# Optimization experiments

Hardware: AMD Instinct MI355X
Metric: run time of the kernel (lower is better)

Reference implementation:

```python
import jax, jax.numpy as jnp
import numpy as np

B, S, D, H = 4, 2048, 512, 8
HD = D // H  # head_size = 64


def setup_inputs() -> dict:
    key = jax.random.key(0)
    ks = jax.random.split(key, 11)
    sd = 1.0 / np.sqrt(D)
    return {
        "q": jax.random.normal(ks[0], (B, S, D), jnp.float32),
        "k": jax.random.normal(ks[1], (B, S, D), jnp.float32),
        "v": jax.random.normal(ks[2], (B, S, D), jnp.float32),
        "Wq": jax.random.normal(ks[3], (D, D), jnp.float32) * sd,
        "bq": jnp.zeros((D,), jnp.float32),
        "Wk": jax.random.normal(ks[4], (D, D), jnp.float32) * sd,
        "bk": jnp.zeros((D,), jnp.float32),
        "Wv": jax.random.normal(ks[5], (D, D), jnp.float32) * sd,
        "bv": jnp.zeros((D,), jnp.float32),
        "Wo": jax.random.normal(ks[6], (D, D), jnp.float32) * sd,
        "bo": jnp.zeros((D,), jnp.float32),
    }


def _split_heads(x):
    # [B,S,D] -> [B,H,S,HD]
    return x.reshape(B, S, H, HD).transpose(0, 2, 1, 3)


def reference(q, k, v, Wq, bq, Wk, bk, Wv, bv, Wo, bo):
    qp = _split_heads(q @ Wq.T + bq)
    kp = _split_heads(k @ Wk.T + bk)
    vp = _split_heads(v @ Wv.T + bv)
    scale = 1.0 / jnp.sqrt(jnp.float32(HD))
    scores = jnp.einsum("bhqd,bhkd->bhqk", qp, kp) * scale  # [B,H,S,S]
    weights = jax.nn.softmax(scores, axis=-1)
    ctx = jnp.einsum("bhqk,bhkd->bhqd", weights, vp)
    ctx = ctx.transpose(0, 2, 1, 3).reshape(B, S, D)
    return ctx @ Wo.T + bo
```

## Files before the change

kernel.cpp:

```cpp
#include <hip/hip_runtime.h>
#include <hip/hip_bf16.h>
#include <stdint.h>

#define BB   4
#define SS   2048
#define DDIM 512
#define HH   8
#define HDIM 64
#define MTOT (BB*SS)
#define QSCALE (0.125f * 1.44269504088896340736f)

typedef __bf16 bf16;
typedef __bf16 bf16x8 __attribute__((ext_vector_type(8)));
typedef float  f32x4  __attribute__((ext_vector_type(4)));

__device__ __forceinline__ f32x4 mfma32(bf16x8 a, bf16x8 b, f32x4 c) {
    return __builtin_amdgcn_mfma_f32_16x16x32_bf16(a, b, c, 0, 0, 0);
}

__device__ __forceinline__ void gload_lds16(const void* g, void* l) {
    __builtin_amdgcn_global_load_lds(
        (__attribute__((address_space(1))) unsigned int*)(uintptr_t)g,
        (__attribute__((address_space(3))) unsigned int*)l,
        16, 0, 0);
}

__device__ __forceinline__ short bf16bits(float f) {
    union { __bf16 h; short s; } u; u.h = (__bf16)f; return u.s;
}

__global__ void cvt_kernel(const float* __restrict__ q, const float* __restrict__ k,
                           const float* __restrict__ v, const float* __restrict__ w0,
                           const float* __restrict__ w1, const float* __restrict__ w2,
                           const float* __restrict__ w3,
                           bf16* __restrict__ dq, bf16* __restrict__ dk,
                           bf16* __restrict__ dv, bf16* __restrict__ dw0,
                           bf16* __restrict__ dw1, bf16* __restrict__ dw2,
                           bf16* __restrict__ dw3) {
    const float* s; bf16* d; int n4;
    switch (blockIdx.y) {
        case 0: s = q;  d = dq;  n4 = (BB*SS*DDIM)/4; break;
        case 1: s = k;  d = dk;  n4 = (BB*SS*DDIM)/4; break;
        case 2: s = v;  d = dv;  n4 = (BB*SS*DDIM)/4; break;
        case 3: s = w0; d = dw0; n4 = (DDIM*DDIM)/4; break;
        case 4: s = w1; d = dw1; n4 = (DDIM*DDIM)/4; break;
        case 5: s = w2; d = dw2; n4 = (DDIM*DDIM)/4; break;
        default: s = w3; d = dw3; n4 = (DDIM*DDIM)/4; break;
    }
    int stride = gridDim.x * blockDim.x;
    for (int i = blockIdx.x * blockDim.x + threadIdx.x; i < n4; i += stride) {
        float4 f = ((const float4*)s)[i];
        union { bf16 h[4]; uint2 u; } o;
        o.h[0] = (bf16)f.x; o.h[1] = (bf16)f.y; o.h[2] = (bf16)f.z; o.h[3] = (bf16)f.w;
        ((uint2*)d)[i] = o.u;
    }
}

#define GEMM_CORE(A_, W_, K_, MB_, NB_)                                          \
    __shared__ bf16 As[2][128 * 32];                                             \
    __shared__ bf16 Bs[2][128 * 32];                                             \
    const int tid = threadIdx.x;                                                 \
    const int w = tid >> 6, lane = tid & 63;                                     \
    const int c15 = lane & 15, quad = lane >> 4;                                 \
    const int mblk = (MB_), nblk = (NB_);                                        \
    const int wm = (w & 1) * 64, wn = (w >> 1) * 64;                             \
    f32x4 acc[4][4] = {};                                                        \
    const bf16* Ab = (A_) + (size_t)mblk * (K_);                                 \
    const bf16* Bb = (W_) + (size_t)nblk * (K_);                                 \
    int goff[2], soff[2];                                                        \
    _Pragma("unroll")                                                            \
    for (int ci = 0; ci < 2; ++ci) {                                             \
        const int s = (w * 2 + ci) * 64 + lane;                 \
        const int kr = s >> 2;                                                   \
        const int c = (s & 3) ^ ((kr >> 1) & 3);                                 \
        goff[ci] = kr * (K_) + c * 8;                                            \
        soff[ci] = s * 8;                                                        \
    }                                                                            \
    _Pragma("unroll")                                                            \
    for (int ci = 0; ci < 2; ++ci) {                                             \
        gload_lds16(Ab + goff[ci], &As[0][soff[ci]]);                            \
        gload_lds16(Bb + goff[ci], &Bs[0][soff[ci]]);                            \
    }                                                                            \
    int bufi = 0;                                                                \
    for (int kt = 0; kt < (K_); kt += 32) {                                      \
        __syncthreads();              \
        if (kt + 32 < (K_)) {                                                    \
            _Pragma("unroll")                                                    \
            for (int ci = 0; ci < 2; ++ci) {                                     \
                gload_lds16(Ab + goff[ci] + kt + 32, &As[bufi ^ 1][soff[ci]]);   \
                gload_lds16(Bb + goff[ci] + kt + 32, &Bs[bufi ^ 1][soff[ci]]);   \
            }                                                                    \
        }                                                                        \
        bf16x8 af[4], bfr[4];                                                    \
        _Pragma("unroll")                                                        \
        for (int i = 0; i < 4; ++i) {                                            \
            const int row = wm + i * 16 + c15;                                   \
            af[i] = *(const bf16x8*)&As[bufi][row * 32 + ((quad ^ ((row >> 1) & 3)) * 8)]; \
        }                                                                        \
        _Pragma("unroll")                                                        \
        for (int j = 0; j < 4; ++j) {                                            \
            const int row = wn + j * 16 + c15;                                   \
            bfr[j] = *(const bf16x8*)&Bs[bufi][row * 32 + ((quad ^ ((row >> 1) & 3)) * 8)]; \
        }                                                                        \
        _Pragma("unroll")                                                        \
        for (int i = 0; i < 4; ++i)                                              \
            _Pragma("unroll")                                                    \
            for (int j = 0; j < 4; ++j)                                          \
                acc[i][j] = mfma32(af[i], bfr[j], acc[i][j]);                    \
        bufi ^= 1;                                                               \
    }

__global__ __launch_bounds__(256, 4)
void proj_gemm(const bf16* __restrict__ qb, const bf16* __restrict__ kb,
               const bf16* __restrict__ vb,
               const bf16* __restrict__ Wq, const bf16* __restrict__ Wk,
               const bf16* __restrict__ Wv,
               const float* __restrict__ bq, const float* __restrict__ bk,
               const float* __restrict__ bv,
               bf16* __restrict__ Qp, bf16* __restrict__ Kp, bf16* __restrict__ Vt2) {
    const int mode = blockIdx.z;
    const bf16* A; const bf16* Wm; const float* bias;
    int mb, nb;
    if (mode == 0)      { A = qb; Wm = Wq; bias = bq; mb = blockIdx.x * 128; nb = blockIdx.y * 128; }
    else if (mode == 1) { A = kb; Wm = Wk; bias = bk; mb = blockIdx.x * 128; nb = blockIdx.y * 128; }
    else {
        const int id = blockIdx.y * 64 + blockIdx.x;
        A = Wv; Wm = vb; bias = bv; mb = (id & 3) * 128; nb = (id >> 2) * 128;
    }
    GEMM_CORE(A, Wm, DDIM, mb, nb)
    if (mode == 2) {
        #pragma unroll
        for (int i = 0; i < 4; ++i) {
            #pragma unroll
            for (int r = 0; r < 4; ++r) {
                const int row = mblk + wm + i * 16 + quad * 4 + r;
                const float bval = bias[row];
                #pragma unroll
                for (int j = 0; j < 4; ++j) {
                    const int col = nblk + wn + j * 16 + c15;
                    const int colp = (col & ~31) + (c15 >> 2) * 8 + (j & 1) * 4 + (c15 & 3);
                    Vt2[(size_t)row * MTOT + colp] = (bf16)(acc[i][j][r] + bval);
                }
            }
        }
    } else {
        #pragma unroll
        for (int j = 0; j < 4; ++j) {
            const int col = nblk + wn + j * 16 + c15;
            const int h = col >> 6, hd = col & 63;
            const float bval = bias[col];
            #pragma unroll
            for (int i = 0; i < 4; ++i) {
                #pragma unroll
                for (int r = 0; r < 4; ++r) {
                    const int row = mblk + wm + i * 16 + quad * 4 + r;
                    const int b = row >> 11, s = row & (SS - 1);
                    float vv = acc[i][j][r] + bval;
                    if (mode == 0) vv *= QSCALE;
                    bf16* dst = (mode == 0) ? Qp : Kp;
                    dst[(((size_t)(b * HH + h)) * SS + s) * HDIM + hd] = (bf16)vv;
                }
            }
        }
    }
}

__global__ __launch_bounds__(256, 4)
void out_gemm(const bf16* __restrict__ A, const bf16* __restrict__ Wo,
              const float* __restrict__ bo, float* __restrict__ Out) {
    __shared__ bf16 As[2][128 * 32];
    __shared__ bf16 Bs[2][64 * 32];
    const int tid = threadIdx.x;
    const int w = tid >> 6, lane = tid & 63;
    const int c15 = lane & 15, quad = lane >> 4;
    const int mblk = blockIdx.x * 128, nblk = blockIdx.y * 64;
    const int wm = (w & 1) * 64, wn = (w >> 1) * 32;
    f32x4 acc[4][2] = {};
    const bf16* Ab = A + (size_t)mblk * DDIM;
    const bf16* Bb = Wo + (size_t)nblk * DDIM;
    int goffA[2], soffA[2];
    #pragma unroll
    for (int ci = 0; ci < 2; ++ci) {
        const int s = (w * 2 + ci) * 64 + lane;
        const int kr = s >> 2;
        const int c = (s & 3) ^ ((kr >> 1) & 3);
        goffA[ci] = kr * DDIM + c * 8;
        soffA[ci] = s * 8;
    }
    const int sB = w * 64 + lane;
    const int krB = sB >> 2;
    const int cB = (sB & 3) ^ ((krB >> 1) & 3);
    const int goffB = krB * DDIM + cB * 8;
    const int soffB = sB * 8;

    #pragma unroll
    for (int ci = 0; ci < 2; ++ci)
        gload_lds16(Ab + goffA[ci], &As[0][soffA[ci]]);
    gload_lds16(Bb + goffB, &Bs[0][soffB]);

    int bufi = 0;
    for (int kt = 0; kt < DDIM; kt += 32) {
        __syncthreads();
        if (kt + 32 < DDIM) {
            #pragma unroll
            for (int ci = 0; ci < 2; ++ci)
                gload_lds16(Ab + goffA[ci] + kt + 32, &As[bufi ^ 1][soffA[ci]]);
            gload_lds16(Bb + goffB + kt + 32, &Bs[bufi ^ 1][soffB]);
        }
        bf16x8 af[4], bfr[2];
        #pragma unroll
        for (int i = 0; i < 4; ++i) {
            const int row = wm + i * 16 + c15;
            af[i] = *(const bf16x8*)&As[bufi][row * 32 + ((quad ^ ((row >> 1) & 3)) * 8)];
        }
        #pragma unroll
        for (int j = 0; j < 2; ++j) {
            const int row = wn + j * 16 + c15;
            bfr[j] = *(const bf16x8*)&Bs[bufi][row * 32 + ((quad ^ ((row >> 1) & 3)) * 8)];
        }
        #pragma unroll
        for (int i = 0; i < 4; ++i)
            #pragma unroll
            for (int j = 0; j < 2; ++j)
                acc[i][j] = mfma32(af[i], bfr[j], acc[i][j]);
        bufi ^= 1;
    }
    #pragma unroll
    for (int j = 0; j < 2; ++j) {
        const int col = nblk + wn + j * 16 + c15;
        const float bval = bo[col];
        #pragma unroll
        for (int i = 0; i < 4; ++i)
            #pragma unroll
            for (int r = 0; r < 4; ++r) {
                const int row = mblk + wm + i * 16 + quad * 4 + r;
                Out[(size_t)row * DDIM + col] = acc[i][j][r] + bval;
            }
    }
}

__global__ __launch_bounds__(256, 2)
void attn_kernel(const bf16* __restrict__ Qp, const bf16* __restrict__ Kp,
                 const bf16* __restrict__ Vt2, bf16* __restrict__ Ctx) {
    __shared__ bf16 Klds[2][128 * 64];
    __shared__ bf16 Vlds[2][64 * 128];

    const int tid = threadIdx.x;
    const int w = tid >> 6, lane = tid & 63;
    const int c15 = lane & 15, quad = lane >> 4;
    const int id = blockIdx.y * 16 + blockIdx.x;
    const int bh = id & 31;
    const int qbase = (id >> 5) * 128;
    const int b = bh >> 3, h = bh & 7;

    const bf16* Qh = Qp + (size_t)bh * SS * HDIM;
    const bf16* Kh = Kp + (size_t)bh * SS * HDIM;
    const bf16* Vh = Vt2 + (size_t)h * HDIM * MTOT + (size_t)b * SS;

    bf16x8 qf[2][2];
    #pragma unroll
    for (int g = 0; g < 2; ++g) {
        const int qrow = qbase + w * 32 + g * 16 + c15;
        qf[g][0] = *(const bf16x8*)&Qh[(size_t)qrow * HDIM + quad * 8];
        qf[g][1] = *(const bf16x8*)&Qh[(size_t)qrow * HDIM + 32 + quad * 8];
    }

    int koff[4], voff[4];
    #pragma unroll
    for (int ci = 0; ci < 4; ++ci) {
        const int s = (w * 4 + ci) * 64 + lane;
        const int kr = s >> 3, kc = (s & 7) ^ (kr & 7);
        koff[ci] = kr * HDIM + kc * 8;
        const int vr = s >> 4, vc = (s & 15) ^ (vr & 15);
        voff[ci] = vr * MTOT + vc * 8;
    }

    union FragS { short s[8]; bf16x8 v; };
    FragS ones8;
    #pragma unroll
    for (int j = 0; j < 8; ++j) ones8.s[j] = (short)0x3F80;

    f32x4 oacc[2][4] = {};
    f32x4 lacc[2] = {};
    const int ksw = c15 & 7;

    #pragma unroll
    for (int ci = 0; ci < 4; ++ci) {
        gload_lds16(Kh + koff[ci], &Klds[0][(w * 4 + ci) * 512]);
        gload_lds16(Vh + voff[ci], &Vlds[0][(w * 4 + ci) * 512]);
    }

    int buf = 0;
    for (int kt = 0; kt < SS; kt += 128) {
        __syncthreads();
        if (kt + 128 < SS) {
            const bf16* Ks = Kh + (size_t)(kt + 128) * HDIM;
            const bf16* Vs = Vh + (kt + 128);
            #pragma unroll
            for (int ci = 0; ci < 4; ++ci) {
                gload_lds16(Ks + koff[ci], &Klds[buf ^ 1][(w * 4 + ci) * 512]);
                gload_lds16(Vs + voff[ci], &Vlds[buf ^ 1][(w * 4 + ci) * 512]);
            }
        }

        FragS paf[2][4];
        #pragma unroll
        for (int nt = 0; nt < 8; ++nt) {
            const int krow = nt * 16 + c15;
            bf16x8 kb0 = *(const bf16x8*)&Klds[buf][(krow * 8 + (quad ^ ksw)) * 8];
            bf16x8 kb1 = *(const bf16x8*)&Klds[buf][(krow * 8 + ((quad + 4) ^ ksw)) * 8];
            #pragma unroll
            for (int g = 0; g < 2; ++g) {
                f32x4 z = {};
                z = mfma32(kb0, qf[g][0], z);
                z = mfma32(kb1, qf[g][1], z);
                const int half = (nt & 1) * 4;
                #pragma unroll
                for (int r = 0; r < 4; ++r)
                    paf[g][nt >> 1].s[half + r] =
                        bf16bits(__builtin_amdgcn_exp2f(z[r]));
            }
        }

        #pragma unroll
        for (int t = 0; t < 4; ++t) {
            bf16x8 vbf[4];
            #pragma unroll
            for (int j = 0; j < 4; ++j) {
                const int row = j * 16 + c15;
                vbf[j] = *(const bf16x8*)&Vlds[buf][row * 128 +
                         (((4 * t + quad) ^ c15) * 8)];
            }
            __builtin_amdgcn_s_setprio(1);
            lacc[0] = mfma32(paf[0][t].v, ones8.v, lacc[0]);
            lacc[1] = mfma32(paf[1][t].v, ones8.v, lacc[1]);
            #pragma unroll
            for (int j = 0; j < 4; ++j) {
                oacc[0][j] = mfma32(paf[0][t].v, vbf[j], oacc[0][j]);
                oacc[1][j] = mfma32(paf[1][t].v, vbf[j], oacc[1][j]);
            }
            __builtin_amdgcn_s_setprio(0);
        }
        buf ^= 1;
    }

    bf16* Cb = Ctx + ((size_t)b * SS) * DDIM + (size_t)h * HDIM;
    #pragma unroll
    for (int g = 0; g < 2; ++g)
        #pragma unroll
        for (int r = 0; r < 4; ++r) {
            const int row = qbase + w * 32 + g * 16 + quad * 4 + r;
            const float inv = 1.0f / lacc[g][r];
            #pragma unroll
            for (int j = 0; j < 4; ++j) {
                const int hd = j * 16 + c15;
                Cb[(size_t)row * DDIM + hd] = (bf16)(oacc[g][j][r] * inv);
            }
        }
}

extern "C" void kernel_launch(void* const* d_in, const int* in_sizes, int n_in,
                              void* d_out, int out_size, void* d_ws, size_t ws_size,
                              hipStream_t stream) {
    const float* q  = (const float*)d_in[0];
    const float* k  = (const float*)d_in[1];
    const float* v  = (const float*)d_in[2];
    const float* Wq = (const float*)d_in[3];
    const float* bq = (const float*)d_in[4];
    const float* Wk = (const float*)d_in[5];
    const float* bk = (const float*)d_in[6];
    const float* Wv = (const float*)d_in[7];
    const float* bv = (const float*)d_in[8];
    const float* Wo = (const float*)d_in[9];
    const float* bo = (const float*)d_in[10];
    float* out = (float*)d_out;

    const size_t SZ_T = (size_t)BB * SS * DDIM * 2;
    const size_t SZ_W = (size_t)DDIM * DDIM * 2;
    char* ws = (char*)d_ws;
    bf16* qb  = (bf16*)(ws + 0 * SZ_T);
    bf16* kb  = (bf16*)(ws + 1 * SZ_T);
    bf16* vb  = (bf16*)(ws + 2 * SZ_T);
    bf16* Wqb = (bf16*)(ws + 3 * SZ_T + 0 * SZ_W);
    bf16* Wkb = (bf16*)(ws + 3 * SZ_T + 1 * SZ_W);
    bf16* Wvb = (bf16*)(ws + 3 * SZ_T + 2 * SZ_W);
    bf16* Wob = (bf16*)(ws + 3 * SZ_T + 3 * SZ_W);
    bf16* Qp  = (bf16*)(ws + 3 * SZ_T + 4 * SZ_W);
    bf16* Kp  = (bf16*)(ws + 4 * SZ_T + 4 * SZ_W);
    bf16* Vt2 = (bf16*)(ws + 5 * SZ_T + 4 * SZ_W);
    bf16* ctx = (bf16*)(ws + 6 * SZ_T + 4 * SZ_W);
    const size_t needed = 7 * SZ_T + 4 * SZ_W;
    if (ws_size < needed) return;

    cvt_kernel<<<dim3(512, 7), 256, 0, stream>>>(q, k, v, Wq, Wk, Wv, Wo,
                                                 qb, kb, vb, Wqb, Wkb, Wvb, Wob);
    proj_gemm<<<dim3(MTOT / 128, DDIM / 128, 3), 256, 0, stream>>>(
        qb, kb, vb, Wqb, Wkb, Wvb, bq, bk, bv, Qp, Kp, Vt2);
    attn_kernel<<<dim3(SS / 128, BB * HH), 256, 0, stream>>>(Qp, Kp, Vt2, ctx);
    out_gemm<<<dim3(MTOT / 128, DDIM / 64), 256, 0, stream>>>(ctx, Wob, bo, out);
}
```

Before: 176.8 us.

## Fuse fp32-to-bf16 activation conversion into projection GEMM loads

The separate conversion pass over q, k and v is removed. The projection GEMM now loads fp32 activations into registers, converts them to bf16 and writes them to LDS, while weights still use direct global-to-LDS DMA. This drops a full write and re-read of three bf16 activation tensors and shrinks the workspace. In exchange, the GEMM reads twice the bytes of activation per tile, uses more registers (launch bounds lowered to 3), and the register-staged path adds latency to the pipeline.

```diff
diff --git a/kernel.cpp b/kernel.cpp
--- a/kernel.cpp
+++ b/kernel.cpp
@@ -29,24 +29,18 @@
     union { __bf16 h; short s; } u; u.h = (__bf16)f; return u.s;
 }
 
-__global__ void cvt_kernel(const float* __restrict__ q, const float* __restrict__ k,
-                           const float* __restrict__ v, const float* __restrict__ w0,
-                           const float* __restrict__ w1, const float* __restrict__ w2,
-                           const float* __restrict__ w3,
-                           bf16* __restrict__ dq, bf16* __restrict__ dk,
-                           bf16* __restrict__ dv, bf16* __restrict__ dw0,
-                           bf16* __restrict__ dw1, bf16* __restrict__ dw2,
-                           bf16* __restrict__ dw3) {
-    const float* s; bf16* d; int n4;
+__global__ void cvt_kernel(const float* __restrict__ w0, const float* __restrict__ w1,
+                           const float* __restrict__ w2, const float* __restrict__ w3,
+                           bf16* __restrict__ d0, bf16* __restrict__ d1,
+                           bf16* __restrict__ d2, bf16* __restrict__ d3) {
+    const float* s; bf16* d;
     switch (blockIdx.y) {
-        case 0: s = q;  d = dq;  n4 = (BB*SS*DDIM)/4; break;
-        case 1: s = k;  d = dk;  n4 = (BB*SS*DDIM)/4; break;
-        case 2: s = v;  d = dv;  n4 = (BB*SS*DDIM)/4; break;
-        case 3: s = w0; d = dw0; n4 = (DDIM*DDIM)/4; break;
-        case 4: s = w1; d = dw1; n4 = (DDIM*DDIM)/4; break;
-        case 5: s = w2; d = dw2; n4 = (DDIM*DDIM)/4; break;
-        default: s = w3; d = dw3; n4 = (DDIM*DDIM)/4; break;
-    }
+        case 0: s = w0; d = d0; break;
+        case 1: s = w1; d = d1; break;
+        case 2: s = w2; d = d2; break;
+        default: s = w3; d = d3; break;
+    }
+    const int n4 = (DDIM * DDIM) / 4;
     int stride = gridDim.x * blockDim.x;
     for (int i = blockIdx.x * blockDim.x + threadIdx.x; i < n4; i += stride) {
         float4 f = ((const float4*)s)[i];
@@ -56,104 +50,152 @@
     }
 }
 
-#define GEMM_CORE(A_, W_, K_, MB_, NB_)                                          \
-    __shared__ bf16 As[2][128 * 32];                                             \
-    __shared__ bf16 Bs[2][128 * 32];                                             \
-    const int tid = threadIdx.x;                                                 \
-    const int w = tid >> 6, lane = tid & 63;                                     \
-    const int c15 = lane & 15, quad = lane >> 4;                                 \
-    const int mblk = (MB_), nblk = (NB_);                                        \
-    const int wm = (w & 1) * 64, wn = (w >> 1) * 64;                             \
-    f32x4 acc[4][4] = {};                                                        \
-    const bf16* Ab = (A_) + (size_t)mblk * (K_);                                 \
-    const bf16* Bb = (W_) + (size_t)nblk * (K_);                                 \
-    int goff[2], soff[2];                                                        \
-    _Pragma("unroll")                                                            \
-    for (int ci = 0; ci < 2; ++ci) {                                             \
-        const int s = (w * 2 + ci) * 64 + lane;                 \
-        const int kr = s >> 2;                                                   \
-        const int c = (s & 3) ^ ((kr >> 1) & 3);                                 \
-        goff[ci] = kr * (K_) + c * 8;                                            \
-        soff[ci] = s * 8;                                                        \
-    }                                                                            \
-    _Pragma("unroll")                                                            \
-    for (int ci = 0; ci < 2; ++ci) {                                             \
-        gload_lds16(Ab + goff[ci], &As[0][soff[ci]]);                            \
-        gload_lds16(Bb + goff[ci], &Bs[0][soff[ci]]);                            \
-    }                                                                            \
-    int bufi = 0;                                                                \
-    for (int kt = 0; kt < (K_); kt += 32) {                                      \
-        __syncthreads();              \
-        if (kt + 32 < (K_)) {                                                    \
-            _Pragma("unroll")                                                    \
-            for (int ci = 0; ci < 2; ++ci) {                                     \
-                gload_lds16(Ab + goff[ci] + kt + 32, &As[bufi ^ 1][soff[ci]]);   \
-                gload_lds16(Bb + goff[ci] + kt + 32, &Bs[bufi ^ 1][soff[ci]]);   \
-            }                                                                    \
-        }                                                                        \
-        bf16x8 af[4], bfr[4];                                                    \
-        _Pragma("unroll")                                                        \
-        for (int i = 0; i < 4; ++i) {                                            \
-            const int row = wm + i * 16 + c15;                                   \
-            af[i] = *(const bf16x8*)&As[bufi][row * 32 + ((quad ^ ((row >> 1) & 3)) * 8)]; \
-        }                                                                        \
-        _Pragma("unroll")                                                        \
-        for (int j = 0; j < 4; ++j) {                                            \
-            const int row = wn + j * 16 + c15;                                   \
-            bfr[j] = *(const bf16x8*)&Bs[bufi][row * 32 + ((quad ^ ((row >> 1) & 3)) * 8)]; \
-        }                                                                        \
-        _Pragma("unroll")                                                        \
-        for (int i = 0; i < 4; ++i)                                              \
-            _Pragma("unroll")                                                    \
-            for (int j = 0; j < 4; ++j)                                          \
-                acc[i][j] = mfma32(af[i], bfr[j], acc[i][j]);                    \
-        bufi ^= 1;                                                               \
-    }
-
-__global__ __launch_bounds__(256, 4)
-void proj_gemm(const bf16* __restrict__ qb, const bf16* __restrict__ kb,
-               const bf16* __restrict__ vb,
+template<bool AF32>
+__device__ __forceinline__ void gemm_mixed(const void* __restrict__ Ap,
+                                           const void* __restrict__ Bp,
+                                           int mblk, int nblk,
+                                           f32x4 (&acc)[4][4],
+                                           bf16 (&As)[2][128 * 32],
+                                           bf16 (&Bs)[2][128 * 32]) {
+    const int tid = threadIdx.x;
+    const int w = tid >> 6, lane = tid & 63;
+    const int c15 = lane & 15, quad = lane >> 4;
+
+    int soff[2], kr_[2], c_[2];
+    #pragma unroll
+    for (int ci = 0; ci < 2; ++ci) {
+        const int s = (w * 2 + ci) * 64 + lane;
+        const int kr = s >> 2;
+        const int c = (s & 3) ^ ((kr >> 1) & 3);
+        kr_[ci] = kr; c_[ci] = c;
+        soff[ci] = s * 8;
+    }
+
+    const float* Rf; const bf16* Db;
+    bf16 (*Rl)[128 * 32]; bf16 (*Dl)[128 * 32];
+    if (AF32) { Rf = (const float*)Ap + (size_t)mblk * DDIM;
+                Db = (const bf16*)Bp + (size_t)nblk * DDIM;
+                Rl = As; Dl = Bs; }
+    else      { Db = (const bf16*)Ap + (size_t)mblk * DDIM;
+                Rf = (const float*)Bp + (size_t)nblk * DDIM;
+                Dl = As; Rl = Bs; }
+
+    float4 ra[2][2];
+#define REG_LOAD(KT_)                                                          \
+    _Pragma("unroll")                                                          \
+    for (int ci = 0; ci < 2; ++ci) {                                           \
+        const float* g = Rf + (size_t)kr_[ci] * DDIM + c_[ci] * 8 + (KT_);     \
+        ra[ci][0] = *(const float4*)(g);                                       \
+        ra[ci][1] = *(const float4*)(g + 4);                                   \
+    }
+#define REG_WRITE(DST_)                                                        \
+    _Pragma("unroll")                                                          \
+    for (int ci = 0; ci < 2; ++ci) {                                           \
+        union { bf16 h[8]; uint4 u; } o;                                       \
+        o.h[0] = (bf16)ra[ci][0].x; o.h[1] = (bf16)ra[ci][0].y;                \
+        o.h[2] = (bf16)ra[ci][0].z; o.h[3] = (bf16)ra[ci][0].w;                \
+        o.h[4] = (bf16)ra[ci][1].x; o.h[5] = (bf16)ra[ci][1].y;                \
+        o.h[6] = (bf16)ra[ci][1].z; o.h[7] = (bf16)ra[ci][1].w;                \
+        *(uint4*)&Rl[DST_][soff[ci]] = o.u;                                    \
+    }
+#define DMA_STAGE(KT_, DST_)                                                   \
+    _Pragma("unroll")                                                          \
+    for (int ci = 0; ci < 2; ++ci)                                             \
+        gload_lds16(Db + (size_t)kr_[ci] * DDIM + c_[ci] * 8 + (KT_),          \
+                    &Dl[DST_][soff[ci]]);
+
+    REG_LOAD(0)
+    DMA_STAGE(0, 0)
+    REG_WRITE(0)
+
+    int bufi = 0;
+    for (int kt = 0; kt < DDIM; kt += 32) {
+        __syncthreads();
+        const bool pre = (kt + 32 < DDIM);
+        if (pre) {
+            REG_LOAD(kt + 32)
+            DMA_STAGE(kt + 32, bufi ^ 1)
+        }
+        bf16x8 af[4], bfr[4];
+        #pragma unroll
+        for (int i = 0; i < 4; ++i) {
+            const int row = (w & 1) * 64 + i * 16 + c15;
+            af[i] = *(const bf16x8*)&As[bufi][row * 32 + ((quad ^ ((row >> 1) & 3)) * 8)];
+        }
+        #pragma unroll
+        for (int j = 0; j < 4; ++j) {
+            const int row = (w >> 1) * 64 + j * 16 + c15;
+            bfr[j] = *(const bf16x8*)&Bs[bufi][row * 32 + ((quad ^ ((row >> 1) & 3)) * 8)];
+        }
+        #pragma unroll
+        for (int i = 0; i < 4; ++i)
+            #pragma unroll
+            for (int j = 0; j < 4; ++j)
+                acc[i][j] = mfma32(af[i], bfr[j], acc[i][j]);
+        if (pre) REG_WRITE(bufi ^ 1)
+        bufi ^= 1;
+    }
+#undef REG_LOAD
+#undef REG_WRITE
+#undef DMA_STAGE
+}
+
+__global__ __launch_bounds__(256, 3)
+void proj_gemm(const float* __restrict__ qf, const float* __restrict__ kf,
+               const float* __restrict__ vf,
                const bf16* __restrict__ Wq, const bf16* __restrict__ Wk,
                const bf16* __restrict__ Wv,
                const float* __restrict__ bq, const float* __restrict__ bk,
                const float* __restrict__ bv,
                bf16* __restrict__ Qp, bf16* __restrict__ Kp, bf16* __restrict__ Vt2) {
+    __shared__ bf16 As[2][128 * 32];
+    __shared__ bf16 Bs[2][128 * 32];
     const int mode = blockIdx.z;
-    const bf16* A; const bf16* Wm; const float* bias;
     int mb, nb;
-    if (mode == 0)      { A = qb; Wm = Wq; bias = bq; mb = blockIdx.x * 128; nb = blockIdx.y * 128; }
-    else if (mode == 1) { A = kb; Wm = Wk; bias = bk; mb = blockIdx.x * 128; nb = blockIdx.y * 128; }
-    else {
+    f32x4 acc[4][4] = {};
+    if (mode == 2) {
         const int id = blockIdx.y * 64 + blockIdx.x;
-        A = Wv; Wm = vb; bias = bv; mb = (id & 3) * 128; nb = (id >> 2) * 128;
-    }
-    GEMM_CORE(A, Wm, DDIM, mb, nb)
+        mb = (id & 3) * 128; nb = (id >> 2) * 128;
+        gemm_mixed<false>(Wv, vf, mb, nb, acc, As, Bs);
+    } else {
+        mb = blockIdx.x * 128; nb = blockIdx.y * 128;
+        gemm_mixed<true>(mode == 0 ? (const void*)qf : (const void*)kf,
+                         mode == 0 ? (const void*)Wq : (const void*)Wk,
+                         mb, nb, acc, As, Bs);
+    }
+
+    const int tid = threadIdx.x;
+    const int w = tid >> 6, lane = tid & 63;
+    const int c15 = lane & 15, quad = lane >> 4;
+    const int wm = (w & 1) * 64, wn = (w >> 1) * 64;
+
     if (mode == 2) {
         #pragma unroll
         for (int i = 0; i < 4; ++i) {
             #pragma unroll
             for (int r = 0; r < 4; ++r) {
-                const int row = mblk + wm + i * 16 + quad * 4 + r;
-                const float bval = bias[row];
+                const int row = mb + wm + i * 16 + quad * 4 + r;
+                const float bval = bv[row];
                 #pragma unroll
                 for (int j = 0; j < 4; ++j) {
-                    const int col = nblk + wn + j * 16 + c15;
+                    const int col = nb + wn + j * 16 + c15;
                     const int colp = (col & ~31) + (c15 >> 2) * 8 + (j & 1) * 4 + (c15 & 3);
                     Vt2[(size_t)row * MTOT + colp] = (bf16)(acc[i][j][r] + bval);
                 }
             }
         }
     } else {
+        const float* bias = (mode == 0) ? bq : bk;
         #pragma unroll
         for (int j = 0; j < 4; ++j) {
-            const int col = nblk + wn + j * 16 + c15;
+            const int col = nb + wn + j * 16 + c15;
             const int h = col >> 6, hd = col & 63;
             const float bval = bias[col];
             #pragma unroll
             for (int i = 0; i < 4; ++i) {
                 #pragma unroll
                 for (int r = 0; r < 4; ++r) {
-                    const int row = mblk + wm + i * 16 + quad * 4 + r;
+                    const int row = mb + wm + i * 16 + quad * 4 + r;
                     const int b = row >> 11, s = row & (SS - 1);
                     float vv = acc[i][j][r] + bval;
                     if (mode == 0) vv *= QSCALE;
@@ -378,24 +420,21 @@
     const size_t SZ_T = (size_t)BB * SS * DDIM * 2;
     const size_t SZ_W = (size_t)DDIM * DDIM * 2;
     char* ws = (char*)d_ws;
-    bf16* qb  = (bf16*)(ws + 0 * SZ_T);
-    bf16* kb  = (bf16*)(ws + 1 * SZ_T);
-    bf16* vb  = (bf16*)(ws + 2 * SZ_T);
-    bf16* Wqb = (bf16*)(ws + 3 * SZ_T + 0 * SZ_W);
-    bf16* Wkb = (bf16*)(ws + 3 * SZ_T + 1 * SZ_W);
-    bf16* Wvb = (bf16*)(ws + 3 * SZ_T + 2 * SZ_W);
-    bf16* Wob = (bf16*)(ws + 3 * SZ_T + 3 * SZ_W);
-    bf16* Qp  = (bf16*)(ws + 3 * SZ_T + 4 * SZ_W);
-    bf16* Kp  = (bf16*)(ws + 4 * SZ_T + 4 * SZ_W);
-    bf16* Vt2 = (bf16*)(ws + 5 * SZ_T + 4 * SZ_W);
-    bf16* ctx = (bf16*)(ws + 6 * SZ_T + 4 * SZ_W);
-    const size_t needed = 7 * SZ_T + 4 * SZ_W;
+    bf16* Wqb = (bf16*)(ws + 0 * SZ_W);
+    bf16* Wkb = (bf16*)(ws + 1 * SZ_W);
+    bf16* Wvb = (bf16*)(ws + 2 * SZ_W);
+    bf16* Wob = (bf16*)(ws + 3 * SZ_W);
+    bf16* Qp  = (bf16*)(ws + 4 * SZ_W + 0 * SZ_T);
+    bf16* Kp  = (bf16*)(ws + 4 * SZ_W + 1 * SZ_T);
+    bf16* Vt2 = (bf16*)(ws + 4 * SZ_W + 2 * SZ_T);
+    bf16* ctx = (bf16*)(ws + 4 * SZ_W + 3 * SZ_T);
+    const size_t needed = 4 * SZ_W + 4 * SZ_T;
     if (ws_size < needed) return;
 
-    cvt_kernel<<<dim3(512, 7), 256, 0, stream>>>(q, k, v, Wq, Wk, Wv, Wo,
-                                                 qb, kb, vb, Wqb, Wkb, Wvb, Wob);
+    cvt_kernel<<<dim3(64, 4), 256, 0, stream>>>(Wq, Wk, Wv, Wo,
+                                                Wqb, Wkb, Wvb, Wob);
     proj_gemm<<<dim3(MTOT / 128, DDIM / 128, 3), 256, 0, stream>>>(
-        qb, kb, vb, Wqb, Wkb, Wvb, bq, bk, bv, Qp, Kp, Vt2);
+        q, k, v, Wqb, Wkb, Wvb, bq, bk, bv, Qp, Kp, Vt2);
     attn_kernel<<<dim3(SS / 128, BB * HH), 256, 0, stream>>>(Qp, Kp, Vt2, ctx);
     out_gemm<<<dim3(MTOT / 128, DDIM / 64), 256, 0, stream>>>(ctx, Wob, bo, out);
 }
```

Result: slower. 182.4 us (+3.1%).
